# Kernel optimization log

Measured on AMD Instinct MI355X. Metric: run time of the kernel, lower is better.

The kernel has to match this reference:

```python
import jax, jax.numpy as jnp
import numpy as np

N = 50000      # nodes
E = 800000     # edges
G = 32         # graphs in batch
C = 10         # num_classes


def _glorot(key, shape):
    lim = float(np.sqrt(6.0 / (shape[0] + shape[1])))
    return jax.random.uniform(key, shape, jnp.float32, -lim, lim)


def setup_inputs() -> dict:
    key = jax.random.key(0)
    ks = jax.random.split(key, 10)
    norm = jax.random.normal(ks[0], (N, 3), jnp.float32)
    pos = jax.random.normal(ks[1], (N, 3), jnp.float32)
    x = jax.random.normal(ks[2], (N, 2), jnp.float32)
    edge_index = jax.random.randint(ks[3], (2, E), 0, N, dtype=jnp.int64)
    batch = jnp.sort(jax.random.randint(ks[4], (N,), 0, G, dtype=jnp.int64))
    return {
        'norm': norm, 'pos': pos, 'x': x,
        'edge_index': edge_index, 'batch': batch,
        'W1': _glorot(ks[5], (8, 64)),   'b1': jnp.zeros((64,), jnp.float32),
        'W2': _glorot(ks[6], (72, 128)), 'b2': jnp.zeros((128,), jnp.float32),
        'W3': _glorot(ks[7], (208, 256)),'b3': jnp.zeros((256,), jnp.float32),
        'Wl': _glorot(ks[8], (256, C)),  'bl': jnp.zeros((C,), jnp.float32),
    }


def gcn_conv(h, W, b, src, dst):
    # GCNConv(normalize=False), edge_weight == 1: out_i = sum_{(j->i)} (h_j @ W) + b
    m = h @ W                      # [N, F_out] dense transform first (cheaper than per-edge)
    msg = m[src]                   # gather per edge [E, F_out]
    agg = jax.ops.segment_sum(msg, dst, num_segments=N)
    return agg + b


def reference(norm, pos, x, edge_index, batch, W1, b1, W2, b2, W3, b3, Wl, bl):
    inp = jnp.concatenate([norm, pos, x], axis=1)      # [N, 8]
    src, dst = edge_index[0], edge_index[1]
    # dropout p=0.2 is identity at inference
    h1 = jax.nn.relu(gcn_conv(inp, W1, b1, src, dst))  # [N, 64]
    h = jnp.concatenate([h1, inp], axis=1)             # [N, 72]
    h2 = jax.nn.relu(gcn_conv(h, W2, b2, src, dst))    # [N, 128]
    h = jnp.concatenate([h, h2, inp], axis=1)          # [N, 208]
    h3 = jax.nn.relu(gcn_conv(h, W3, b3, src, dst))    # [N, 256]
    pooled = jax.ops.segment_max(h3, batch, num_segments=G)  # global_max_pool [G, 256]
    logits = pooled @ Wl + bl
    out = jax.nn.log_softmax(logits, axis=1)
    pred = jax.nn.softmax(out, axis=1)
    return (out, pred)
```

## Files before the change

kernel.cpp:

```cpp
#include <hip/hip_runtime.h>
#include <hip/hip_bf16.h>

#define NN 50000
#define EE 800000
#define GG 32
#define SCB 512

#define BSH 6
#define NBUK 782
#define NBLK1 256
#define EPB (EE / NBLK1)
#define MH (NBUK * NBLK1)
#define NB2 ((MH + SCB - 1) / SCB)
#define CAP2 2048

#define NSL 8
#define CHN 256
#define NCH ((NN + CHN - 1) / CHN)

#define B_PREP ((NN + 255) / 256)
#define TOTW (64 * 32 + 128 * 96 + 256 * 224)
#define B_WTP ((TOTW + 255) / 256)

using short8 = __attribute__((ext_vector_type(8))) short;
using f32x4  = __attribute__((ext_vector_type(4))) float;

__device__ __forceinline__ ushort f2bf(float f) {
    __hip_bfloat16 hb = __float2bfloat16(f);
    return *reinterpret_cast<ushort*>(&hb);
}

__device__ __forceinline__ void acc8(uint4 v, float* a) {
    a[0] += __uint_as_float(v.x << 16); a[1] += __uint_as_float(v.x & 0xffff0000u);
    a[2] += __uint_as_float(v.y << 16); a[3] += __uint_as_float(v.y & 0xffff0000u);
    a[4] += __uint_as_float(v.z << 16); a[5] += __uint_as_float(v.z & 0xffff0000u);
    a[6] += __uint_as_float(v.w << 16); a[7] += __uint_as_float(v.w & 0xffff0000u);
}

__device__ __forceinline__ void wtp_one(const float* W, ushort* Wt, int K, int F,
                                        int KPAD, int mode, int idx) {
    int n = idx / KPAD, k = idx - n * KPAD;
    float v = 0.f;
    if (k < K) {
        int ko = k;
        if (mode == 2) ko = (k < 8) ? (k + 64) : (k - 8);
        v = W[(size_t)ko * F + n];
        if (mode == 1 && ko >= 64 && ko < 72) v += W[(size_t)(ko + 136) * F + n];
    }
    Wt[idx] = f2bf(v);
}


__global__ __launch_bounds__(256) void setup_k(
        const int* __restrict__ edst, int* __restrict__ hist,
        const float* __restrict__ nrm, const float* __restrict__ pos,
        const float* __restrict__ x, ushort* __restrict__ inpb,
        const float* __restrict__ W1, ushort* __restrict__ Wt1,
        const float* __restrict__ W2, ushort* __restrict__ Wt2,
        const float* __restrict__ W3, ushort* __restrict__ Wt3,
        float* __restrict__ pooled) {
    int blk = blockIdx.x, tid = threadIdx.x;
    if (blk < NBLK1) {
        __shared__ uint cnt[NBUK];
        for (int i = tid; i < NBUK; i += 256) cnt[i] = 0;
        __syncthreads();
        int base = blk * EPB;
        for (int i = tid; i < EPB; i += 256)
            atomicAdd(&cnt[(uint)edst[base + i] >> BSH], 1u);
        __syncthreads();
        for (int b = tid; b < NBUK; b += 256)
            hist[(size_t)b * NBLK1 + blk] = (int)cnt[b];
    } else if (blk < NBLK1 + B_PREP) {
        int i = (blk - NBLK1) * 256 + tid;
        if (i < NN) {
            float v[8];
            v[0] = nrm[i * 3]; v[1] = nrm[i * 3 + 1]; v[2] = nrm[i * 3 + 2];
            v[3] = pos[i * 3]; v[4] = pos[i * 3 + 1]; v[5] = pos[i * 3 + 2];
            v[6] = x[i * 2];   v[7] = x[i * 2 + 1];
            uint4 d;
            d.x = (uint)f2bf(v[0]) | ((uint)f2bf(v[1]) << 16);
            d.y = (uint)f2bf(v[2]) | ((uint)f2bf(v[3]) << 16);
            d.z = (uint)f2bf(v[4]) | ((uint)f2bf(v[5]) << 16);
            d.w = (uint)f2bf(v[6]) | ((uint)f2bf(v[7]) << 16);
            *reinterpret_cast<uint4*>(&inpb[(size_t)i * 8]) = d;
        }
    } else if (blk < NBLK1 + B_PREP + B_WTP) {
        int idx = (blk - NBLK1 - B_PREP) * 256 + tid;
        if (idx < 64 * 32) { wtp_one(W1, Wt1, 8, 64, 32, 0, idx); return; }
        idx -= 64 * 32;
        if (idx < 128 * 96) { wtp_one(W2, Wt2, 72, 128, 96, 2, idx); return; }
        idx -= 128 * 96;
        if (idx < 256 * 224) wtp_one(W3, Wt3, 200, 256, 224, 1, idx);
    } else {
        for (int q = tid; q < GG * 256; q += 256) pooled[q] = 0.f;
    }
}


__global__ __launch_bounds__(SCB) void scan1_k(const int* __restrict__ in,
                                               int* __restrict__ bsum, int M) {
    __shared__ int ws[SCB / 64];
    int tid = threadIdx.x, lane = tid & 63, w = tid >> 6;
    int i = blockIdx.x * SCB + tid;
    int s = (i < M) ? in[i] : 0;
    #pragma unroll
    for (int off = 32; off >= 1; off >>= 1) s += __shfl_down(s, off, 64);
    if (lane == 0) ws[w] = s;
    __syncthreads();
    if (tid == 0) {
        int t = 0;
        #pragma unroll
        for (int j = 0; j < SCB / 64; j++) t += ws[j];
        bsum[blockIdx.x] = t;
    }
}

__global__ __launch_bounds__(64) void scan2g_k(int* __restrict__ bsum, int nb) {
    int lane = threadIdx.x;
    int carry = 0;
    for (int base = 0; base < nb; base += 64) {
        int v = (base + lane < nb) ? bsum[base + lane] : 0;
        int s = v;
        #pragma unroll
        for (int off = 1; off < 64; off <<= 1) {
            int t = __shfl_up(s, off, 64);
            if (lane >= off) s += t;
        }
        if (base + lane < nb) bsum[base + lane] = carry + s - v;
        carry += __shfl(s, 63, 64);
    }
}

__global__ __launch_bounds__(SCB) void scan3g_k(const int* __restrict__ in,
                                                const int* __restrict__ bsum,
                                                int* __restrict__ out, int M) {
    __shared__ int ws[SCB / 64];
    int tid = threadIdx.x, lane = tid & 63, w = tid >> 6;
    int i = blockIdx.x * SCB + tid;
    int v = (i < M) ? in[i] : 0;
    int s = v;
    #pragma unroll
    for (int off = 1; off < 64; off <<= 1) {
        int t = __shfl_up(s, off, 64);
        if (lane >= off) s += t;
    }
    if (lane == 63) ws[w] = s;
    __syncthreads();
    if (w == 0 && lane < SCB / 64) {
        int t = ws[lane];
        #pragma unroll
        for (int off = 1; off < SCB / 64; off <<= 1) {
            int u = __shfl_up(t, off, 64);
            if (lane >= off) t += u;
        }
        ws[lane] = t;
    }
    __syncthreads();
    if (i < M) out[i] = (w ? ws[w - 1] : 0) + s - v + bsum[blockIdx.x];
}


__global__ __launch_bounds__(256) void bsort1_k(const int* __restrict__ esrc,
                                                const int* __restrict__ edst,
                                                const int* __restrict__ ofs,
                                                uint* __restrict__ packed) {
    __shared__ uint cnt[1024];
    __shared__ uint lofs0[1024];
    __shared__ uint goff[NBUK];
    __shared__ uint stage[EPB];
    __shared__ uint wsum[4];
    int tid = threadIdx.x, blk = blockIdx.x;
    int lane = tid & 63, wv = tid >> 6;

    for (int i = tid; i < 1024; i += 256) cnt[i] = 0;
    __syncthreads();
    int base = blk * EPB;
    for (int i = tid; i < EPB; i += 256)
        atomicAdd(&cnt[(uint)edst[base + i] >> BSH], 1u);
    __syncthreads();

    uint c0 = cnt[tid * 4 + 0], c1 = cnt[tid * 4 + 1];
    uint c2 = cnt[tid * 4 + 2], c3 = cnt[tid * 4 + 3];
    uint ts = c0 + c1 + c2 + c3;
    uint sc = ts;
    #pragma unroll
    for (int off = 1; off < 64; off <<= 1) {
        uint t = __shfl_up(sc, off, 64);
        if (lane >= off) sc += t;
    }
    if (lane == 63) wsum[wv] = sc;
    __syncthreads();
    uint wbase = 0;
    for (int j = 0; j < wv; j++) wbase += wsum[j];
    uint run = wbase + sc - ts;
    lofs0[tid * 4 + 0] = run;
    lofs0[tid * 4 + 1] = run + c0;
    lofs0[tid * 4 + 2] = run + c0 + c1;
    lofs0[tid * 4 + 3] = run + c0 + c1 + c2;
    cnt[tid * 4 + 0] = run;
    cnt[tid * 4 + 1] = run + c0;
    cnt[tid * 4 + 2] = run + c0 + c1;
    cnt[tid * 4 + 3] = run + c0 + c1 + c2;
    for (int b = tid; b < NBUK; b += 256)
        goff[b] = (uint)ofs[(size_t)b * NBLK1 + blk];
    __syncthreads();

    for (int i = tid; i < EPB; i += 256) {
        int d = edst[base + i];
        uint b = (uint)d >> BSH;
        uint pos = atomicAdd(&cnt[b], 1u);
        stage[pos] = (b << 22) | ((uint)(d & 63) << 16) | (uint)esrc[base + i];
    }
    __syncthreads();

    for (int i = tid; i < EPB; i += 256) {
        uint p = stage[i];
        uint b = p >> 22;
        packed[goff[b] + ((uint)i - lofs0[b])] = p & 0x3FFFFFu;
    }
}


__global__ __launch_bounds__(256) void bsort2_k(const uint* __restrict__ packed,
                                                const int* __restrict__ ofs,
                                                ushort* __restrict__ col,
                                                int* __restrict__ rowptr) {
    __shared__ uint buf[CAP2];
    __shared__ ushort srt[CAP2];
    __shared__ uint fcnt[64], fofs[64];
    int b = blockIdx.x, tid = threadIdx.x;
    uint g0 = (uint)ofs[(size_t)b * NBLK1];
    uint g1 = (b + 1 < NBUK) ? (uint)ofs[(size_t)(b + 1) * NBLK1] : (uint)EE;
    uint n = g1 - g0;
    if (tid < 64) fcnt[tid] = 0;
    __syncthreads();
    for (uint i = tid; i < n; i += 256) {
        uint p = packed[g0 + i];
        buf[i] = p;
        atomicAdd(&fcnt[(p >> 16) & 63], 1u);
    }
    __syncthreads();
    if (tid < 64) {
        uint v = fcnt[tid], s = v;
        #pragma unroll
        for (int off = 1; off < 64; off <<= 1) {
            uint t = __shfl_up(s, off, 64);
            if (tid >= off) s += t;
        }
        uint e0 = s - v;
        fofs[tid] = e0;
        int node = (b << BSH) + tid;
        if (node < NN) rowptr[node] = (int)(g0 + e0);
    }
    if (b == NBUK - 1 && tid == 0) rowptr[NN] = EE;
    __syncthreads();
    for (uint i = tid; i < n; i += 256) {
        uint p = buf[i];
        uint pos = atomicAdd(&fofs[(p >> 16) & 63], 1u);
        srt[pos] = (ushort)(p & 0xFFFFu);
    }
    __syncthreads();
    for (uint i = tid; i < n; i += 256) col[g0 + i] = srt[i];
}


template <int K, int KPAD, int LDA, int F, int WPA, int WPB, int WG, bool SLICEOUT>
__global__ __launch_bounds__(512) void layer_k(
        const ushort* __restrict__ preA, const ushort* __restrict__ preB,
        const ushort* __restrict__ gsrc,
        const int* __restrict__ rowptr, const ushort* __restrict__ col,
        const ushort* __restrict__ Wt, const float* __restrict__ bias,
        ushort* __restrict__ aggout, ushort* __restrict__ out, int N) {
    constexpr int WPRE = WPA + WPB;
    constexpr int NU4 = WG / 8;
    constexpr int TPN = (NU4 < 8) ? NU4 : 8;
    static_assert(NU4 / TPN >= 1, "");
    constexpr int U4PT = NU4 / TPN;
    constexpr int KS = KPAD / 32;
    constexpr int FW = F / 4;
    constexpr int NT = FW / 16;

    __shared__ ushort At[64 * LDA];

    const int node0 = blockIdx.x * 64;
    const int tid = threadIdx.x;
    const int lane = tid & 63;
    const int wv = tid >> 6;
    const int wm = wv & 1;
    const int wn = wv >> 1;

    {
        int m = tid / TPN;
        int j = tid - m * TPN;
        if (m < 64) {
            int i = node0 + m;
            float ga0[U4PT * 8], ga1[U4PT * 8];
            #pragma unroll
            for (int q = 0; q < U4PT * 8; q++) { ga0[q] = 0.f; ga1[q] = 0.f; }
            if (i < N) {
                int e0 = rowptr[i], e1 = rowptr[i + 1];
                int e = e0;
                for (; e + 1 < e1; e += 2) {
                    int s0 = col[e], s1 = col[e + 1];
                    #pragma unroll
                    for (int u = 0; u < U4PT; u++) {
                        uint4 v0 = *reinterpret_cast<const uint4*>(
                            &gsrc[(size_t)s0 * WG + (j * U4PT + u) * 8]);
                        uint4 v1 = *reinterpret_cast<const uint4*>(
                            &gsrc[(size_t)s1 * WG + (j * U4PT + u) * 8]);
                        acc8(v0, ga0 + u * 8);
                        acc8(v1, ga1 + u * 8);
                    }
                }
                if (e < e1) {
                    int s0 = col[e];
                    #pragma unroll
                    for (int u = 0; u < U4PT; u++) {
                        uint4 v0 = *reinterpret_cast<const uint4*>(
                            &gsrc[(size_t)s0 * WG + (j * U4PT + u) * 8]);
                        acc8(v0, ga0 + u * 8);
                    }
                }
            }
            #pragma unroll
            for (int u = 0; u < U4PT; u++) {
                uint4 o;
                o.x = (uint)f2bf(ga0[u*8+0] + ga1[u*8+0]) | ((uint)f2bf(ga0[u*8+1] + ga1[u*8+1]) << 16);
                o.y = (uint)f2bf(ga0[u*8+2] + ga1[u*8+2]) | ((uint)f2bf(ga0[u*8+3] + ga1[u*8+3]) << 16);
                o.z = (uint)f2bf(ga0[u*8+4] + ga1[u*8+4]) | ((uint)f2bf(ga0[u*8+5] + ga1[u*8+5]) << 16);
                o.w = (uint)f2bf(ga0[u*8+6] + ga1[u*8+6]) | ((uint)f2bf(ga0[u*8+7] + ga1[u*8+7]) << 16);
                *reinterpret_cast<uint4*>(&At[m * LDA + WPRE + (j * U4PT + u) * 8]) = o;
                if (aggout != nullptr && i < N)
                    *reinterpret_cast<uint4*>(&aggout[(size_t)i * WG + (j * U4PT + u) * 8]) = o;
            }
        }
    }

    if constexpr (WPRE > 0) {
        constexpr int NP = WPRE / 8;
        for (int idx = tid; idx < 64 * NP; idx += 512) {
            int m = idx / NP, q = idx - m * NP;
            int i = node0 + m;
            uint4 v = make_uint4(0, 0, 0, 0);
            if (i < N) {
                int c = q * 8;
                if (c < WPA) v = *reinterpret_cast<const uint4*>(&preA[(size_t)i * WPA + c]);
                else v = *reinterpret_cast<const uint4*>(&preB[(size_t)i * WPB + (c - WPA)]);
            }
            *reinterpret_cast<uint4*>(&At[m * LDA + q * 8]) = v;
        }
    }
    {
        constexpr int PAD = LDA - K;
        for (int idx = tid; idx < 64 * PAD; idx += 512) {
            int m = idx / PAD, k = K + (idx - m * PAD);
            At[m * LDA + k] = 0;
        }
    }
    __syncthreads();

    const int r15 = lane & 15, kg = lane >> 4;

    short8 a[2][KS];
    #pragma unroll
    for (int s = 0; s < 2; s++)
        #pragma unroll
        for (int kc = 0; kc < KS; kc++)
            a[s][kc] = *reinterpret_cast<const short8*>(
                &At[(wm * 32 + s * 16 + r15) * LDA + kg * 8 + kc * 32]);

    f32x4 acc[2][NT];
    #pragma unroll
    for (int s = 0; s < 2; s++)
        #pragma unroll
        for (int nt = 0; nt < NT; nt++) acc[s][nt] = (f32x4){0.f, 0.f, 0.f, 0.f};

    const ushort* wbase = &Wt[(size_t)(wn * FW + r15) * KPAD + kg * 8];
    #pragma unroll
    for (int nt = 0; nt < NT; nt++) {
        short8 b[KS];
        #pragma unroll
        for (int kc = 0; kc < KS; kc++)
            b[kc] = *reinterpret_cast<const short8*>(
                wbase + (size_t)nt * 16 * KPAD + kc * 32);
        #pragma unroll
        for (int kc = 0; kc < KS; kc++) {
            acc[0][nt] = __builtin_amdgcn_mfma_f32_16x16x32_bf16(a[0][kc], b[kc], acc[0][nt], 0, 0, 0);
            acc[1][nt] = __builtin_amdgcn_mfma_f32_16x16x32_bf16(a[1][kc], b[kc], acc[1][nt], 0, 0, 0);
        }
    }

    #pragma unroll
    for (int s = 0; s < 2; s++)
        #pragma unroll
        for (int nt = 0; nt < NT; nt++) {
            int colg = wn * FW + nt * 16 + r15;
            float bv = bias[colg];
            #pragma unroll
            for (int reg = 0; reg < 4; reg++) {
                int row = node0 + wm * 32 + s * 16 + kg * 4 + reg;
                if (row < N) {
                    float v = fmaxf(acc[s][nt][reg] + bv, 0.f);
                    if constexpr (SLICEOUT)
                        out[((size_t)(colg >> 4) * NN + row) * 16 + (colg & 15)] = f2bf(v);
                    else
                        out[(size_t)row * F + colg] = f2bf(v);
                }
            }
        }
}


__global__ __launch_bounds__(512) void agg3s_k(const int* __restrict__ rowptr,
                                               const ushort* __restrict__ col,
                                               const ushort* __restrict__ h2s,
                                               ushort* __restrict__ aggh2s, int N) {
    int slice = blockIdx.x % NSL;
    int chunk = blockIdx.x / NSL;
    int m = chunk * CHN + (threadIdx.x >> 1);
    int h = threadIdx.x & 1;
    if (m >= N) return;
    const ushort* src = h2s + ((size_t)slice * NN) * 16 + h * 8;
    float a0[8] = {0,0,0,0,0,0,0,0};
    float a1[8] = {0,0,0,0,0,0,0,0};
    float a2[8] = {0,0,0,0,0,0,0,0};
    float a3[8] = {0,0,0,0,0,0,0,0};
    int e0 = rowptr[m], e1 = rowptr[m + 1];
    int e = e0;
    for (; e + 3 < e1; e += 4) {
        int s0 = col[e], s1 = col[e + 1], s2 = col[e + 2], s3 = col[e + 3];
        uint4 v0 = *reinterpret_cast<const uint4*>(&src[(size_t)s0 * 16]);
        uint4 v1 = *reinterpret_cast<const uint4*>(&src[(size_t)s1 * 16]);
        uint4 v2 = *reinterpret_cast<const uint4*>(&src[(size_t)s2 * 16]);
        uint4 v3 = *reinterpret_cast<const uint4*>(&src[(size_t)s3 * 16]);
        acc8(v0, a0); acc8(v1, a1); acc8(v2, a2); acc8(v3, a3);
    }
    for (; e < e1; e++) {
        uint4 v0 = *reinterpret_cast<const uint4*>(&src[(size_t)col[e] * 16]);
        acc8(v0, a0);
    }
    uint4 o;
    o.x = (uint)f2bf((a0[0]+a1[0])+(a2[0]+a3[0])) | ((uint)f2bf((a0[1]+a1[1])+(a2[1]+a3[1])) << 16);
    o.y = (uint)f2bf((a0[2]+a1[2])+(a2[2]+a3[2])) | ((uint)f2bf((a0[3]+a1[3])+(a2[3]+a3[3])) << 16);
    o.z = (uint)f2bf((a0[4]+a1[4])+(a2[4]+a3[4])) | ((uint)f2bf((a0[5]+a1[5])+(a2[5]+a3[5])) << 16);
    o.w = (uint)f2bf((a0[6]+a1[6])+(a2[6]+a3[6])) | ((uint)f2bf((a0[7]+a1[7])+(a2[7]+a3[7])) << 16);
    *reinterpret_cast<uint4*>(&aggh2s[((size_t)slice * NN + m) * 16 + h * 8]) = o;
}


__global__ __launch_bounds__(512) void layer3_k(
        const ushort* __restrict__ aggh1, const ushort* __restrict__ agg1,
        const ushort* __restrict__ aggh2s,
        const ushort* __restrict__ Wt, const float* __restrict__ bias,
        const int* __restrict__ batch, float* __restrict__ pooled, int N) {
    constexpr int KPAD = 224, LDA = 264, F = 256;
    constexpr int KS = KPAD / 32;
    constexpr int FW = F / 4;
    constexpr int NT = FW / 16;

    __shared__ ushort At[64 * LDA];
    __shared__ int batchv[64];

    const int node0 = blockIdx.x * 64;
    const int tid = threadIdx.x;
    const int lane = tid & 63;
    const int wv = tid >> 6;
    const int wm = wv & 1;
    const int wn = wv >> 1;

    for (int idx = tid; idx < 64 * 8; idx += 512) {
        int m = idx >> 3, q = idx & 7;
        int i = node0 + m;
        uint4 v = make_uint4(0, 0, 0, 0);
        if (i < N) v = *reinterpret_cast<const uint4*>(&aggh1[(size_t)i * 64 + q * 8]);
        *reinterpret_cast<uint4*>(&At[m * LDA + q * 8]) = v;
    }
    for (int idx = tid; idx < 64; idx += 512) {
        int m = idx;
        int i = node0 + m;
        uint4 v = make_uint4(0, 0, 0, 0);
        if (i < N) v = *reinterpret_cast<const uint4*>(&agg1[(size_t)i * 8]);
        *reinterpret_cast<uint4*>(&At[m * LDA + 64]) = v;
    }
    for (int idx = tid; idx < 64 * 16; idx += 512) {
        int m = idx >> 4;
        int s = (idx >> 1) & 7, h = idx & 1;
        int i = node0 + m;
        uint4 v = make_uint4(0, 0, 0, 0);
        if (i < N) v = *reinterpret_cast<const uint4*>(
            &aggh2s[((size_t)s * NN + i) * 16 + h * 8]);
        *reinterpret_cast<uint4*>(&At[m * LDA + 72 + s * 16 + h * 8]) = v;
    }
    for (int idx = tid; idx < 64 * 3; idx += 512) {
        int m = idx / 3, q = idx - m * 3;
        *reinterpret_cast<uint4*>(&At[m * LDA + 200 + q * 8]) = make_uint4(0, 0, 0, 0);
    }
    if (tid < 64) batchv[tid] = (node0 + tid < N) ? batch[node0 + tid] : -1;
    __syncthreads();

    const int r15 = lane & 15, kg = lane >> 4;

    short8 a[2][KS];
    #pragma unroll
    for (int s = 0; s < 2; s++)
        #pragma unroll
        for (int kc = 0; kc < KS; kc++)
            a[s][kc] = *reinterpret_cast<const short8*>(
                &At[(wm * 32 + s * 16 + r15) * LDA + kg * 8 + kc * 32]);

    f32x4 acc[2][NT];
    #pragma unroll
    for (int s = 0; s < 2; s++)
        #pragma unroll
        for (int nt = 0; nt < NT; nt++) acc[s][nt] = (f32x4){0.f, 0.f, 0.f, 0.f};

    const ushort* wbase = &Wt[(size_t)(wn * FW + r15) * KPAD + kg * 8];
    #pragma unroll
    for (int nt = 0; nt < NT; nt++) {
        short8 b[KS];
        #pragma unroll
        for (int kc = 0; kc < KS; kc++)
            b[kc] = *reinterpret_cast<const short8*>(
                wbase + (size_t)nt * 16 * KPAD + kc * 32);
        #pragma unroll
        for (int kc = 0; kc < KS; kc++) {
            acc[0][nt] = __builtin_amdgcn_mfma_f32_16x16x32_bf16(a[0][kc], b[kc], acc[0][nt], 0, 0, 0);
            acc[1][nt] = __builtin_amdgcn_mfma_f32_16x16x32_bf16(a[1][kc], b[kc], acc[1][nt], 0, 0, 0);
        }
    }

    __syncthreads();
    ushort* H3 = At;
    #pragma unroll
    for (int s = 0; s < 2; s++)
        #pragma unroll
        for (int nt = 0; nt < NT; nt++) {
            int colg = wn * FW + nt * 16 + r15;
            float bv = bias[colg];
            #pragma unroll
            for (int reg = 0; reg < 4; reg++) {
                int m = wm * 32 + s * 16 + kg * 4 + reg;
                float v = fmaxf(acc[s][nt][reg] + bv, 0.f);
                H3[m * 256 + colg] = f2bf(v);
            }
        }
    __syncthreads();
    int nvalid = min(64, N - node0);
    int c = tid & 255, half = tid >> 8;
    int m0 = half * 32;
    int m1 = min(m0 + 32, nvalid);
    int curg = -1;
    float cm = 0.f;
    for (int m = m0; m < m1; m++) {
        int g = batchv[m];
        if (g != curg) {
            if (curg >= 0)
                atomicMax(reinterpret_cast<int*>(&pooled[curg * 256 + c]),
                          __float_as_int(cm));
            curg = g;
            cm = 0.f;
        }
        cm = fmaxf(cm, __uint_as_float((uint)H3[m * 256 + c] << 16));
    }
    if (curg >= 0)
        atomicMax(reinterpret_cast<int*>(&pooled[curg * 256 + c]),
                  __float_as_int(cm));
}


__global__ __launch_bounds__(320) void head_k(const float* __restrict__ pooled,
                                              const float* __restrict__ Wl,
                                              const float* __restrict__ bl,
                                              float* __restrict__ out) {
    __shared__ float lg[GG][10];
    __shared__ float lse[GG];
    int t = threadIdx.x;
    int g = t / 10, c = t % 10;
    float acc = bl[c];
    for (int k = 0; k < 256; k++) acc = fmaf(pooled[g * 256 + k], Wl[k * 10 + c], acc);
    lg[g][c] = acc;
    __syncthreads();
    if (c == 0) {
        float mx = -1e30f;
        for (int j = 0; j < 10; j++) mx = fmaxf(mx, lg[g][j]);
        float s = 0.f;
        for (int j = 0; j < 10; j++) s += expf(lg[g][j] - mx);
        lse[g] = mx + logf(s);
    }
    __syncthreads();
    float o = acc - lse[g];
    out[g * 10 + c] = o;
    out[320 + g * 10 + c] = expf(o);
}


extern "C" void kernel_launch(void* const* d_in, const int* in_sizes, int n_in,
                              void* d_out, int out_size, void* d_ws, size_t ws_size,
                              hipStream_t stream) {
    const int N = NN, E = EE;
    const float* nrm = (const float*)d_in[0];
    const float* pos = (const float*)d_in[1];
    const float* x   = (const float*)d_in[2];
    const int* ei    = (const int*)d_in[3];
    const int* batch = (const int*)d_in[4];
    const float* W1 = (const float*)d_in[5];
    const float* b1 = (const float*)d_in[6];
    const float* W2 = (const float*)d_in[7];
    const float* b2 = (const float*)d_in[8];
    const float* W3 = (const float*)d_in[9];
    const float* b3 = (const float*)d_in[10];
    const float* Wl = (const float*)d_in[11];
    const float* bl = (const float*)d_in[12];

    const int* esrc = ei;
    const int* edst = ei + E;

    char* w = (char*)d_ws;
    auto carve = [&](size_t bytes) {
        void* p = (void*)w;
        w += (bytes + 255) & ~(size_t)255;
        return p;
    };
    int* hist     = (int*)carve((size_t)MH * 4);
    int* ofs      = (int*)carve((size_t)MH * 4);
    int* bsum     = (int*)carve((size_t)NB2 * 4);
    uint* packed  = (uint*)carve((size_t)E * 4);
    int* rowptr   = (int*)carve((size_t)(N + 1) * 4);
    ushort* col   = (ushort*)carve((size_t)E * 2);
    ushort* inpb  = (ushort*)carve((size_t)N * 8 * 2);
    ushort* agg1  = (ushort*)carve((size_t)N * 8 * 2);
    ushort* h1    = (ushort*)carve((size_t)N * 64 * 2);
    ushort* aggh1 = (ushort*)carve((size_t)N * 64 * 2);
    ushort* h2s   = (ushort*)carve((size_t)NSL * N * 16 * 2);
    ushort* aggh2s= (ushort*)carve((size_t)NSL * N * 16 * 2);
    ushort* Wt1   = (ushort*)carve((size_t)64 * 32 * 2);
    ushort* Wt2   = (ushort*)carve((size_t)128 * 96 * 2);
    ushort* Wt3   = (ushort*)carve((size_t)256 * 224 * 2);
    float* pooled = (float*)carve((size_t)GG * 256 * 4);

    setup_k<<<NBLK1 + B_PREP + B_WTP + 1, 256, 0, stream>>>(
        edst, hist, nrm, pos, x, inpb, W1, Wt1, W2, Wt2, W3, Wt3, pooled);

    scan1_k<<<NB2, SCB, 0, stream>>>(hist, bsum, MH);
    scan2g_k<<<1, 64, 0, stream>>>(bsum, NB2);
    scan3g_k<<<NB2, SCB, 0, stream>>>(hist, bsum, ofs, MH);
    bsort1_k<<<NBLK1, 256, 0, stream>>>(esrc, edst, ofs, packed);
    bsort2_k<<<NBUK, 256, 0, stream>>>(packed, ofs, col, rowptr);

    layer_k<8, 32, 40, 64, 0, 0, 8, false><<<NBUK, 512, 0, stream>>>(
        nullptr, nullptr, inpb, rowptr, col, Wt1, b1, agg1, h1, N);

    layer_k<72, 96, 104, 128, 8, 0, 64, true><<<NBUK, 512, 0, stream>>>(
        agg1, nullptr, h1, rowptr, col, Wt2, b2, aggh1, h2s, N);

    agg3s_k<<<NCH * NSL, 512, 0, stream>>>(rowptr, col, h2s, aggh2s, N);

    layer3_k<<<NBUK, 512, 0, stream>>>(aggh1, agg1, aggh2s, Wt3, b3, batch, pooled, N);

    head_k<<<1, 320, 0, stream>>>(pooled, Wl, bl, (float*)d_out);
}
```

Measured before the change: 149.5 us.

## Replace sliced h2 layout with row-major layout and 8-thread-per-node gather

Layer 2 now writes its output row-major ([N,128]) instead of as 8 column slices of 16 features, and the layer-3 aggregation kernel is rewritten so 8 threads per node each gather 32 contiguous bytes per edge. The sliced layout existed to keep each slice's gather working set cache-resident. The new layout trades that locality for fully contiguous 256-byte row reads, fewer col/rowptr reloads (once per node instead of once per slice) and simpler layer-2 stores and layer-3 loads. It risks more L2 misses because the whole 12.8 MB h2 array is touched at random.

```diff
diff --git a/kernel.cpp b/kernel.cpp
--- a/kernel.cpp
+++ b/kernel.cpp
@@ -13,10 +13,6 @@
 #define MH (NBUK * NBLK1)
 #define NB2 ((MH + SCB - 1) / SCB)
 #define CAP2 2048
-
-#define NSL 8
-#define CHN 256
-#define NCH ((NN + CHN - 1) / CHN)
 
 #define B_PREP ((NN + 255) / 256)
 #define TOTW (64 * 32 + 128 * 96 + 256 * 224)
@@ -264,7 +260,7 @@
 }
 
 
-template <int K, int KPAD, int LDA, int F, int WPA, int WPB, int WG, bool SLICEOUT>
+template <int K, int KPAD, int LDA, int F, int WPA, int WPB, int WG>
 __global__ __launch_bounds__(512) void layer_k(
         const ushort* __restrict__ preA, const ushort* __restrict__ preB,
         const ushort* __restrict__ gsrc,
@@ -274,7 +270,6 @@
     constexpr int WPRE = WPA + WPB;
     constexpr int NU4 = WG / 8;
     constexpr int TPN = (NU4 < 8) ? NU4 : 8;
-    static_assert(NU4 / TPN >= 1, "");
     constexpr int U4PT = NU4 / TPN;
     constexpr int KS = KPAD / 32;
     constexpr int FW = F / 4;
@@ -401,56 +396,58 @@
                 int row = node0 + wm * 32 + s * 16 + kg * 4 + reg;
                 if (row < N) {
                     float v = fmaxf(acc[s][nt][reg] + bv, 0.f);
-                    if constexpr (SLICEOUT)
-                        out[((size_t)(colg >> 4) * NN + row) * 16 + (colg & 15)] = f2bf(v);
-                    else
-                        out[(size_t)row * F + colg] = f2bf(v);
+                    out[(size_t)row * F + colg] = f2bf(v);
                 }
             }
         }
 }
 
 
-__global__ __launch_bounds__(512) void agg3s_k(const int* __restrict__ rowptr,
-                                               const ushort* __restrict__ col,
-                                               const ushort* __restrict__ h2s,
-                                               ushort* __restrict__ aggh2s, int N) {
-    int slice = blockIdx.x % NSL;
-    int chunk = blockIdx.x / NSL;
-    int m = chunk * CHN + (threadIdx.x >> 1);
-    int h = threadIdx.x & 1;
+__global__ __launch_bounds__(256) void gather3_k(const int* __restrict__ rowptr,
+                                                 const ushort* __restrict__ col,
+                                                 const ushort* __restrict__ h2,
+                                                 ushort* __restrict__ aggh2, int N) {
+    int m = blockIdx.x * 32 + (threadIdx.x >> 3);
+    int j = threadIdx.x & 7;
     if (m >= N) return;
-    const ushort* src = h2s + ((size_t)slice * NN) * 16 + h * 8;
-    float a0[8] = {0,0,0,0,0,0,0,0};
-    float a1[8] = {0,0,0,0,0,0,0,0};
-    float a2[8] = {0,0,0,0,0,0,0,0};
-    float a3[8] = {0,0,0,0,0,0,0,0};
+    const size_t jo = (size_t)j * 16;
+    float a0[16], a1[16];
+    #pragma unroll
+    for (int q = 0; q < 16; q++) { a0[q] = 0.f; a1[q] = 0.f; }
     int e0 = rowptr[m], e1 = rowptr[m + 1];
     int e = e0;
-    for (; e + 3 < e1; e += 4) {
-        int s0 = col[e], s1 = col[e + 1], s2 = col[e + 2], s3 = col[e + 3];
-        uint4 v0 = *reinterpret_cast<const uint4*>(&src[(size_t)s0 * 16]);
-        uint4 v1 = *reinterpret_cast<const uint4*>(&src[(size_t)s1 * 16]);
-        uint4 v2 = *reinterpret_cast<const uint4*>(&src[(size_t)s2 * 16]);
-        uint4 v3 = *reinterpret_cast<const uint4*>(&src[(size_t)s3 * 16]);
-        acc8(v0, a0); acc8(v1, a1); acc8(v2, a2); acc8(v3, a3);
-    }
-    for (; e < e1; e++) {
-        uint4 v0 = *reinterpret_cast<const uint4*>(&src[(size_t)col[e] * 16]);
-        acc8(v0, a0);
-    }
-    uint4 o;
-    o.x = (uint)f2bf((a0[0]+a1[0])+(a2[0]+a3[0])) | ((uint)f2bf((a0[1]+a1[1])+(a2[1]+a3[1])) << 16);
-    o.y = (uint)f2bf((a0[2]+a1[2])+(a2[2]+a3[2])) | ((uint)f2bf((a0[3]+a1[3])+(a2[3]+a3[3])) << 16);
-    o.z = (uint)f2bf((a0[4]+a1[4])+(a2[4]+a3[4])) | ((uint)f2bf((a0[5]+a1[5])+(a2[5]+a3[5])) << 16);
-    o.w = (uint)f2bf((a0[6]+a1[6])+(a2[6]+a3[6])) | ((uint)f2bf((a0[7]+a1[7])+(a2[7]+a3[7])) << 16);
-    *reinterpret_cast<uint4*>(&aggh2s[((size_t)slice * NN + m) * 16 + h * 8]) = o;
-}
-
-
-__global__ __launch_bounds__(512) void layer3_k(
+    for (; e + 1 < e1; e += 2) {
+        int s0 = col[e], s1 = col[e + 1];
+        uint4 v00 = *reinterpret_cast<const uint4*>(&h2[(size_t)s0 * 128 + jo]);
+        uint4 v01 = *reinterpret_cast<const uint4*>(&h2[(size_t)s0 * 128 + jo + 8]);
+        uint4 v10 = *reinterpret_cast<const uint4*>(&h2[(size_t)s1 * 128 + jo]);
+        uint4 v11 = *reinterpret_cast<const uint4*>(&h2[(size_t)s1 * 128 + jo + 8]);
+        acc8(v00, a0); acc8(v01, a0 + 8);
+        acc8(v10, a1); acc8(v11, a1 + 8);
+    }
+    if (e < e1) {
+        int s0 = col[e];
+        uint4 v00 = *reinterpret_cast<const uint4*>(&h2[(size_t)s0 * 128 + jo]);
+        uint4 v01 = *reinterpret_cast<const uint4*>(&h2[(size_t)s0 * 128 + jo + 8]);
+        acc8(v00, a0); acc8(v01, a0 + 8);
+    }
+    uint4 o0, o1;
+    o0.x = (uint)f2bf(a0[0] + a1[0])  | ((uint)f2bf(a0[1] + a1[1]) << 16);
+    o0.y = (uint)f2bf(a0[2] + a1[2])  | ((uint)f2bf(a0[3] + a1[3]) << 16);
+    o0.z = (uint)f2bf(a0[4] + a1[4])  | ((uint)f2bf(a0[5] + a1[5]) << 16);
+    o0.w = (uint)f2bf(a0[6] + a1[6])  | ((uint)f2bf(a0[7] + a1[7]) << 16);
+    o1.x = (uint)f2bf(a0[8] + a1[8])  | ((uint)f2bf(a0[9] + a1[9]) << 16);
+    o1.y = (uint)f2bf(a0[10] + a1[10]) | ((uint)f2bf(a0[11] + a1[11]) << 16);
+    o1.z = (uint)f2bf(a0[12] + a1[12]) | ((uint)f2bf(a0[13] + a1[13]) << 16);
+    o1.w = (uint)f2bf(a0[14] + a1[14]) | ((uint)f2bf(a0[15] + a1[15]) << 16);
+    *reinterpret_cast<uint4*>(&aggh2[(size_t)m * 128 + jo]) = o0;
+    *reinterpret_cast<uint4*>(&aggh2[(size_t)m * 128 + jo + 8]) = o1;
+}
+
+
+__global__ __launch_bounds__(512) void layer3b_k(
         const ushort* __restrict__ aggh1, const ushort* __restrict__ agg1,
-        const ushort* __restrict__ aggh2s,
+        const ushort* __restrict__ aggh2,
         const ushort* __restrict__ Wt, const float* __restrict__ bias,
         const int* __restrict__ batch, float* __restrict__ pooled, int N) {
     constexpr int KPAD = 224, LDA = 264, F = 256;
@@ -483,13 +480,11 @@
         *reinterpret_cast<uint4*>(&At[m * LDA + 64]) = v;
     }
     for (int idx = tid; idx < 64 * 16; idx += 512) {
-        int m = idx >> 4;
-        int s = (idx >> 1) & 7, h = idx & 1;
+        int m = idx >> 4, q = idx & 15;
         int i = node0 + m;
         uint4 v = make_uint4(0, 0, 0, 0);
-        if (i < N) v = *reinterpret_cast<const uint4*>(
-            &aggh2s[((size_t)s * NN + i) * 16 + h * 8]);
-        *reinterpret_cast<uint4*>(&At[m * LDA + 72 + s * 16 + h * 8]) = v;
+        if (i < N) v = *reinterpret_cast<const uint4*>(&aggh2[(size_t)i * 128 + q * 8]);
+        *reinterpret_cast<uint4*>(&At[m * LDA + 72 + q * 8]) = v;
     }
     for (int idx = tid; idx < 64 * 3; idx += 512) {
         int m = idx / 3, q = idx - m * 3;
@@ -631,8 +626,8 @@
     ushort* agg1  = (ushort*)carve((size_t)N * 8 * 2);
     ushort* h1    = (ushort*)carve((size_t)N * 64 * 2);
     ushort* aggh1 = (ushort*)carve((size_t)N * 64 * 2);
-    ushort* h2s   = (ushort*)carve((size_t)NSL * N * 16 * 2);
-    ushort* aggh2s= (ushort*)carve((size_t)NSL * N * 16 * 2);
+    ushort* h2    = (ushort*)carve((size_t)N * 128 * 2);
+    ushort* aggh2 = (ushort*)carve((size_t)N * 128 * 2);
     ushort* Wt1   = (ushort*)carve((size_t)64 * 32 * 2);
     ushort* Wt2   = (ushort*)carve((size_t)128 * 96 * 2);
     ushort* Wt3   = (ushort*)carve((size_t)256 * 224 * 2);
@@ -647,15 +642,15 @@
     bsort1_k<<<NBLK1, 256, 0, stream>>>(esrc, edst, ofs, packed);
     bsort2_k<<<NBUK, 256, 0, stream>>>(packed, ofs, col, rowptr);
 
-    layer_k<8, 32, 40, 64, 0, 0, 8, false><<<NBUK, 512, 0, stream>>>(
+    layer_k<8, 32, 40, 64, 0, 0, 8><<<NBUK, 512, 0, stream>>>(
         nullptr, nullptr, inpb, rowptr, col, Wt1, b1, agg1, h1, N);
 
-    layer_k<72, 96, 104, 128, 8, 0, 64, true><<<NBUK, 512, 0, stream>>>(
-        agg1, nullptr, h1, rowptr, col, Wt2, b2, aggh1, h2s, N);
-
-    agg3s_k<<<NCH * NSL, 512, 0, stream>>>(rowptr, col, h2s, aggh2s, N);
-
-    layer3_k<<<NBUK, 512, 0, stream>>>(aggh1, agg1, aggh2s, Wt3, b3, batch, pooled, N);
+    layer_k<72, 96, 104, 128, 8, 0, 64><<<NBUK, 512, 0, stream>>>(
+        agg1, nullptr, h1, rowptr, col, Wt2, b2, aggh1, h2, N);
+
+    gather3_k<<<(N + 31) / 32, 256, 0, stream>>>(rowptr, col, h2, aggh2, N);
+
+    layer3b_k<<<NBUK, 512, 0, stream>>>(aggh1, agg1, aggh2, Wt3, b3, batch, pooled, N);
 
     head_k<<<1, 320, 0, stream>>>(pooled, Wl, bl, (float*)d_out);
 }
```

New measurement: 142.6 us. -4.6%, faster.
